# Kernel tuning notes

Hardware: AMD Instinct MI355X
Metric: run time of the kernel (lower is better)

The kernel has to match this reference:

```python
import jax, jax.numpy as jnp
import numpy as np

N = 1048576        # number of time samples (rays)
V = 32             # num_videos
D = 32             # embedding_dim
F = 6              # num_frequencies
K = 2 * F + 1      # basis size: [1, sin(2^j*pi*t), cos(2^j*pi*t)]


def setup_inputs() -> dict:
    key = jax.random.key(0)
    k1, k2, k3 = jax.random.split(key, 3)
    times = jax.random.uniform(k1, (N, 1), dtype=jnp.float32)
    video_ids = jax.random.randint(k2, (N, 1), 0, V, dtype=jnp.int32)
    weights = jax.random.normal(k3, (V, D, K), dtype=jnp.float32)
    return {"times": times, "video_ids": video_ids, "weights": weights}


def _fourier_basis(t):
    # t: [N] -> [N, K] with basis [1, sin(2^j pi t), cos(2^j pi t)] j=0..F-1
    freqs = (2.0 ** jnp.arange(F, dtype=t.dtype)) * jnp.pi  # [F]
    ang = t[:, None] * freqs                                # [N, F]
    return jnp.concatenate(
        [jnp.ones_like(t)[:, None], jnp.sin(ang), jnp.cos(ang)], axis=-1
    )


def reference(times, video_ids, weights):
    shp = times.shape
    t = times.reshape(-1)                       # [N]
    vid = video_ids.reshape(-1).astype(jnp.int32)  # [N]
    basis = _fourier_basis(t)                   # [N, K]
    w = weights[vid]                            # gather: [N, D, K]
    emb = jnp.einsum('ndk,nk->nd', w, basis)    # [N, D]
    return emb.reshape((*shp[:-1], -1))
```

## Files before the change

### kernel.cpp

```cpp
#include <hip/hip_runtime.h>
#include <hip/hip_fp16.h>

#define NRAYS 1048576
#define NV 32
#define ND 32
#define NF 6
#define NK 13

typedef _Float16 h2 __attribute__((ext_vector_type(2)));
typedef float f4 __attribute__((ext_vector_type(4)));

__device__ __forceinline__ float fdot2acc(h2 a, h2 b, float c) {
#if __has_builtin(__builtin_amdgcn_fdot2)
    return __builtin_amdgcn_fdot2(a, b, c, false);
#else
    return c + (float)a.x * (float)b.x + (float)a.y * (float)b.y;
#endif
}

__device__ __forceinline__ h2 pack2(float a, float b) {
#if __has_builtin(__builtin_amdgcn_cvt_pkrtz)
    return __builtin_bit_cast(h2, __builtin_amdgcn_cvt_pkrtz(a, b));
#else
    h2 r; r.x = (_Float16)a; r.y = (_Float16)b; return r;
#endif
}

__device__ __forceinline__ float hwsin(float rev) {
#if __has_builtin(__builtin_amdgcn_sinf)
    return __builtin_amdgcn_sinf(rev);
#else
    return __sinf(6.28318530717958647692f * rev);
#endif
}
__device__ __forceinline__ float hwcos(float rev) {
#if __has_builtin(__builtin_amdgcn_cosf)
    return __builtin_amdgcn_cosf(rev);
#else
    return __cosf(6.28318530717958647692f * rev);
#endif
}

__device__ __forceinline__ void make_basis(float t, h2 bp[7]) {
    float sv[NF], cv[NF];
    sv[0] = hwsin(0.5f * t);
    cv[0] = hwcos(0.5f * t);
#pragma unroll
    for (int j = 1; j < NF; ++j) {
        float sj = sv[j - 1], cj = cv[j - 1];
        sv[j] = 2.f * sj * cj;
        cv[j] = fmaf(-2.f * sj, sj, 1.f);
    }
    bp[0] = pack2(1.0f, sv[0]);
    bp[1] = pack2(sv[1], sv[2]);
    bp[2] = pack2(sv[3], sv[4]);
    bp[3] = pack2(sv[5], cv[0]);
    bp[4] = pack2(cv[1], cv[2]);
    bp[5] = pack2(cv[3], cv[4]);
    bp[6] = pack2(cv[5], 0.0f);
}

__global__ void pack_weights_kernel(const float* __restrict__ weights,
                                    unsigned* __restrict__ wpack)
{
    int j = blockIdx.x * 256 + threadIdx.x;
    if (j >= NV * 7 * 32) return;
    int v = j / 224;
    int r = j - v * 224;
    int i = r >> 5;
    int c = r & 31;
    int pos = c >> 2;
    int e = c & 3;
    int q = pos ^ (v & 7);
    int d = 4 * q + e;
    float w0 = weights[v * (ND * NK) + d * NK + 2 * i];
    float w1 = (2 * i + 1 < NK) ? weights[v * (ND * NK) + d * NK + 2 * i + 1] : 0.f;
    wpack[j] = __builtin_bit_cast(unsigned, pack2(w0, w1));
}

__global__ __launch_bounds__(256, 5) void VideoEmbedding_kernel(
    const float* __restrict__ times,
    const int* __restrict__ vids,
    const unsigned* __restrict__ wpack,
    float* __restrict__ out)
{
    __shared__ _Float16 wl[NV * 7 * ND * 2];

    const int tid = threadIdx.x;
    {
        const uint4* src = reinterpret_cast<const uint4*>(wpack);
        uint4* dst = reinterpret_cast<uint4*>(wl);
#pragma unroll
        for (int j = 0; j < 7; ++j)
            dst[tid + j * 256] = src[tid + j * 256];
    }
    __syncthreads();

    const int q = tid & 7;
    const int gs = (gridDim.x * 256) >> 3;
    int ray = ((blockIdx.x * 256) + tid) >> 3;

    float t0, t1, t2;
    int v0, v1, v2;
    t0 = times[ray]; v0 = vids[ray];
    int rr = min(ray + gs, NRAYS - 1);
    t1 = times[rr]; v1 = vids[rr];
    rr = min(ray + 2 * gs, NRAYS - 1);
    t2 = times[rr]; v2 = vids[rr];

    uint4 wA[7], wB[7];

    {
        const unsigned base = (unsigned)v0 * 448u + (unsigned)(q ^ (v0 & 7)) * 8u;
#pragma unroll
        for (int i = 0; i < 7; ++i)
            wA[i] = *reinterpret_cast<const uint4*>(&wl[base + i * 64]);
    }

#define STAGE(WCUR, WNEXT)                                                    \
    {                                                                         \
                                               \
        rr = min(ray + 3 * gs, NRAYS - 1);                                    \
        const float t3 = times[rr];                                           \
        const int v3 = vids[rr];                                              \
                                    \
        {                                                                     \
            const unsigned nb =                                               \
                (unsigned)v1 * 448u + (unsigned)(q ^ (v1 & 7)) * 8u;          \
            _Pragma("unroll")                                                 \
            for (int i = 0; i < 7; ++i)                                       \
                WNEXT[i] = *reinterpret_cast<const uint4*>(&wl[nb + i * 64]); \
        }                                                                     \
                                   \
        {                                                                     \
            h2 bp[7];                                                         \
            make_basis(t0, bp);                                               \
            float a0 = 0.f, a1 = 0.f, a2 = 0.f, a3 = 0.f;                     \
            _Pragma("unroll")                                                 \
            for (int i = 0; i < 7; ++i) {                                     \
                a0 = fdot2acc(__builtin_bit_cast(h2, WCUR[i].x), bp[i], a0);  \
                a1 = fdot2acc(__builtin_bit_cast(h2, WCUR[i].y), bp[i], a1);  \
                a2 = fdot2acc(__builtin_bit_cast(h2, WCUR[i].z), bp[i], a2);  \
                a3 = fdot2acc(__builtin_bit_cast(h2, WCUR[i].w), bp[i], a3);  \
            }                                                                 \
            f4 res;                                                           \
            res.x = a0; res.y = a1; res.z = a2; res.w = a3;                   \
            reinterpret_cast<f4*>(out)[(size_t)ray * 8 + q] = res;            \
        }                                                                     \
        ray += gs;                                                            \
        if (ray >= NRAYS) break;                                              \
        t0 = t1; t1 = t2; t2 = t3;                                            \
        v0 = v1; v1 = v2; v2 = v3;                                            \
    }

    while (true) {
        STAGE(wA, wB)
        STAGE(wB, wA)
    }
#undef STAGE
}

extern "C" void kernel_launch(void* const* d_in, const int* in_sizes, int n_in,
                              void* d_out, int out_size, void* d_ws, size_t ws_size,
                              hipStream_t stream) {
    const float* times = (const float*)d_in[0];
    const int* vids = (const int*)d_in[1];
    const float* weights = (const float*)d_in[2];
    float* out = (float*)d_out;
    unsigned* wpack = (unsigned*)d_ws;

    hipLaunchKernelGGL(pack_weights_kernel, dim3(28), dim3(256), 0, stream,
                       weights, wpack);
    hipLaunchKernelGGL(VideoEmbedding_kernel, dim3(1280), dim3(256), 0, stream,
                       times, vids, wpack, out);
}
```

Measured before the change: 34.98 us.

## Stage per-block times and video ids in shared memory with fixed 512-ray tiles

Replaces the grid-stride persistent loop with fixed 512-ray tiles per block (2048 blocks). Each block loads its times and video ids with coalesced loads into shared memory together with the packed weights, then loops over 16 ray-groups reading them from LDS. This removes the scattered per-ray global loads for times and ids inside the loop. In exchange, every block reloads the 28 KB weight table and there are more blocks to launch. The code assumes NRAYS is divisible by 512 * 2048, which holds here.

After: 33.77 us (median of 3 runs). 3.4% less time.

```diff
diff --git a/kernel.cpp b/kernel.cpp
--- a/kernel.cpp
+++ b/kernel.cpp
@@ -85,79 +85,80 @@
     float* __restrict__ out)
 {
     __shared__ _Float16 wl[NV * 7 * ND * 2];
+    __shared__ float s_t[512];
+    __shared__ unsigned char s_v[512];
 
     const int tid = threadIdx.x;
+    const int rbase = blockIdx.x * 512;
+
+    uint4 wst[7];
     {
         const uint4* src = reinterpret_cast<const uint4*>(wpack);
+#pragma unroll
+        for (int j = 0; j < 7; ++j)
+            wst[j] = src[tid + j * 256];
+    }
+    const float t0 = times[rbase + tid];
+    const float t1 = times[rbase + 256 + tid];
+    const int v0i = vids[rbase + tid];
+    const int v1i = vids[rbase + 256 + tid];
+
+    {
         uint4* dst = reinterpret_cast<uint4*>(wl);
 #pragma unroll
         for (int j = 0; j < 7; ++j)
-            dst[tid + j * 256] = src[tid + j * 256];
+            dst[tid + j * 256] = wst[j];
     }
+    s_t[tid] = t0;
+    s_t[tid + 256] = t1;
+    s_v[tid] = (unsigned char)v0i;
+    s_v[tid + 256] = (unsigned char)v1i;
     __syncthreads();
 
     const int q = tid & 7;
-    const int gs = (gridDim.x * 256) >> 3;
-    int ray = ((blockIdx.x * 256) + tid) >> 3;
-
-    float t0, t1, t2;
-    int v0, v1, v2;
-    t0 = times[ray]; v0 = vids[ray];
-    int rr = min(ray + gs, NRAYS - 1);
-    t1 = times[rr]; v1 = vids[rr];
-    rr = min(ray + 2 * gs, NRAYS - 1);
-    t2 = times[rr]; v2 = vids[rr];
+    const int g = tid >> 3;
 
     uint4 wA[7], wB[7];
-
     {
-        const unsigned base = (unsigned)v0 * 448u + (unsigned)(q ^ (v0 & 7)) * 8u;
+        const int v = s_v[g];
+        const unsigned b = (unsigned)v * 448u + (unsigned)(q ^ (v & 7)) * 8u;
 #pragma unroll
         for (int i = 0; i < 7; ++i)
-            wA[i] = *reinterpret_cast<const uint4*>(&wl[base + i * 64]);
+            wA[i] = *reinterpret_cast<const uint4*>(&wl[b + i * 64]);
     }
 
-#define STAGE(WCUR, WNEXT)                                                    \
+#define ITER(P, WCUR, WNEXT)                                                  \
     {                                                                         \
-                                               \
-        rr = min(ray + 3 * gs, NRAYS - 1);                                    \
-        const float t3 = times[rr];                                           \
-        const int v3 = vids[rr];                                              \
-                                    \
-        {                                                                     \
+        if ((P) < 15) {                    \
+            const int nv = s_v[((P) + 1) * 32 + g];                           \
             const unsigned nb =                                               \
-                (unsigned)v1 * 448u + (unsigned)(q ^ (v1 & 7)) * 8u;          \
+                (unsigned)nv * 448u + (unsigned)(q ^ (nv & 7)) * 8u;          \
             _Pragma("unroll")                                                 \
             for (int i = 0; i < 7; ++i)                                       \
                 WNEXT[i] = *reinterpret_cast<const uint4*>(&wl[nb + i * 64]); \
         }                                                                     \
-                                   \
-        {                                                                     \
-            h2 bp[7];                                                         \
-            make_basis(t0, bp);                                               \
-            float a0 = 0.f, a1 = 0.f, a2 = 0.f, a3 = 0.f;                     \
-            _Pragma("unroll")                                                 \
-            for (int i = 0; i < 7; ++i) {                                     \
-                a0 = fdot2acc(__builtin_bit_cast(h2, WCUR[i].x), bp[i], a0);  \
-                a1 = fdot2acc(__builtin_bit_cast(h2, WCUR[i].y), bp[i], a1);  \
-                a2 = fdot2acc(__builtin_bit_cast(h2, WCUR[i].z), bp[i], a2);  \
-                a3 = fdot2acc(__builtin_bit_cast(h2, WCUR[i].w), bp[i], a3);  \
-            }                                                                 \
-            f4 res;                                                           \
-            res.x = a0; res.y = a1; res.z = a2; res.w = a3;                   \
-            reinterpret_cast<f4*>(out)[(size_t)ray * 8 + q] = res;            \
+        const float t = s_t[(P) * 32 + g];                                    \
+        h2 bp[7];                                                             \
+        make_basis(t, bp);                                                    \
+        float a0 = 0.f, a1 = 0.f, a2 = 0.f, a3 = 0.f;                         \
+        _Pragma("unroll")                                                     \
+        for (int i = 0; i < 7; ++i) {                                         \
+            a0 = fdot2acc(__builtin_bit_cast(h2, WCUR[i].x), bp[i], a0);      \
+            a1 = fdot2acc(__builtin_bit_cast(h2, WCUR[i].y), bp[i], a1);      \
+            a2 = fdot2acc(__builtin_bit_cast(h2, WCUR[i].z), bp[i], a2);      \
+            a3 = fdot2acc(__builtin_bit_cast(h2, WCUR[i].w), bp[i], a3);      \
         }                                                                     \
-        ray += gs;                                                            \
-        if (ray >= NRAYS) break;                                              \
-        t0 = t1; t1 = t2; t2 = t3;                                            \
-        v0 = v1; v1 = v2; v2 = v3;                                            \
+        f4 res;                                                               \
+        res.x = a0; res.y = a1; res.z = a2; res.w = a3;                       \
+        reinterpret_cast<f4*>(out)[(size_t)(rbase + (P) * 32 + g) * 8 + q] =  \
+            res;                                                              \
     }
 
-    while (true) {
-        STAGE(wA, wB)
-        STAGE(wB, wA)
+    for (int p = 0; p < 16; p += 2) {
+        ITER(p, wA, wB)
+        ITER(p + 1, wB, wA)
     }
-#undef STAGE
+#undef ITER
 }
 
 extern "C" void kernel_launch(void* const* d_in, const int* in_sizes, int n_in,
@@ -171,6 +172,6 @@
 
     hipLaunchKernelGGL(pack_weights_kernel, dim3(28), dim3(256), 0, stream,
                        weights, wpack);
-    hipLaunchKernelGGL(VideoEmbedding_kernel, dim3(1280), dim3(256), 0, stream,
+    hipLaunchKernelGGL(VideoEmbedding_kernel, dim3(2048), dim3(256), 0, stream,
                        times, vids, wpack, out);
 }
```
